# Optimization experiments

Measured on AMD Instinct MI355X. Metric: run time of the kernel, lower is better.

## Reference

```python
import jax, jax.numpy as jnp
import numpy as np
import math

N = 100000      # num nodes
D = 5           # fixed degree per node (<=5 -> exact Shapley enumeration path)
F_IN = 128
F_OUT = 128


def _subset_coeffs(d):
    """Exact Shapley subset-enumeration coefficients for a node with d neighbors.
    For subset S (mask m_k over neighbor slots, |S|=s):
      marginal = (sum_S + x_i)/(s+1) - (sum_S/s if s>0 else 0)   [since mean_S]
      weight   = s! (d-s)! / (d+1)!
    contrib = sum_k w_k*marginal_k = einsum(sum_S, c1) + x_i * sum(c2)
    """
    k = np.arange(2 ** d)
    masks = ((k[:, None] >> np.arange(d)) & 1).astype(np.float32)  # [2^d, d]
    s = masks.sum(axis=1)
    fact = np.vectorize(math.factorial)
    w = (fact(s.astype(np.int64)) * fact((d - s).astype(np.int64))
         / math.factorial(d + 1)).astype(np.float32)
    c1 = np.where(s > 0, w * (1.0 / (s + 1.0) - 1.0 / np.maximum(s, 1.0)), 0.0).astype(np.float32)
    c2 = (w / (s + 1.0)).astype(np.float32)
    return jnp.asarray(masks), jnp.asarray(c1), jnp.asarray(float(c2.sum()))


def setup_inputs() -> dict:
    key = jax.random.key(0)
    k1, k2, k3 = jax.random.split(key, 3)
    x = jax.random.normal(k1, (N, F_IN), dtype=jnp.float32)
    # fixed-degree graph: node i owns edges [i*D, (i+1)*D); row sorted
    row = jnp.repeat(jnp.arange(N, dtype=jnp.int32), D)
    col = jax.random.randint(k2, (N * D,), 0, N, dtype=jnp.int32)
    edge_index = jnp.stack([row, col])  # [2, N*D]
    W = jax.random.normal(k3, (F_OUT, F_IN), dtype=jnp.float32) / np.float32(np.sqrt(F_IN))
    return {"x": x, "edge_index": edge_index, "W": W}


def reference(x, edge_index, W):
    n = x.shape[0]
    col = edge_index[1]
    d = col.shape[0] // n
    nbrs = col.reshape(n, d)          # neighbors of node i (row is sorted, fixed degree)
    xn = x[nbrs]                      # [n, d, f] gathered neighbor features
    masks, c1, c2_sum = _subset_coeffs(d)
    # per-subset neighbor-feature sums: [n, 2^d, f]
    sum_S = jnp.einsum('kd,ndf->nkf', masks, xn)
    contrib = jnp.einsum('nkf,k->nf', sum_S, c1) + x * c2_sum
    shapley = x + contrib             # x_i + Shapley contribution
    out = jax.nn.relu(shapley @ W.T)  # Linear(bias=False) + relu
    return out
```

## Files before the change

kernel.cpp:

```cpp
#include <hip/hip_runtime.h>
#include <hip/hip_bf16.h>

typedef __attribute__((ext_vector_type(8))) short short8;
typedef __attribute__((ext_vector_type(4))) float f32x4;

#define DEG 5
#define FDIM 128
#define MT 64
#define NTHR 256
#define LROW 136

__device__ __forceinline__ short f2bf(float f) {
    unsigned u = __builtin_bit_cast(unsigned, f);
    unsigned r = (u + 0x7fffu + ((u >> 16) & 1u)) >> 16;
    return (short)(r & 0xffffu);
}

__global__ __launch_bounds__(NTHR) void shapley_gnn_kernel(
    const float* __restrict__ x,
    const int* __restrict__ col,
    const float* __restrict__ W,
    float* __restrict__ out,
    int n)
{
    __shared__ short sS[MT * LROW];
    __shared__ short sW[FDIM * LROW];
    __shared__ int sIdx[MT * DEG];

    const int tid = threadIdx.x;
    const int base = blockIdx.x * MT;

    for (int i = tid; i < MT * DEG; i += NTHR) {
        int e = base * DEG + i;
        sIdx[i] = (e < n * DEG) ? col[e] : 0;
    }

    for (int t = tid; t < FDIM * 16; t += NTHR) {
        int r = t >> 4;
        int c = t & 15;
        const float4* wp = reinterpret_cast<const float4*>(W + r * FDIM + c * 8);
        float4 w0 = wp[0];
        float4 w1 = wp[1];
        short8 v;
        v[0] = f2bf(w0.x); v[1] = f2bf(w0.y); v[2] = f2bf(w0.z); v[3] = f2bf(w0.w);
        v[4] = f2bf(w1.x); v[5] = f2bf(w1.y); v[6] = f2bf(w1.z); v[7] = f2bf(w1.w);
        *reinterpret_cast<short8*>(&sW[r * LROW + c * 8]) = v;
    }
    __syncthreads();

    const float CSELF = 1.4083333333333334f;
    const float ALPHA = -0.04833333333333333f;

    for (int t = tid; t < MT * 16; t += NTHR) {
        int m = t >> 4;
        int c = t & 15;
        int node = base + m;
        float a0, a1, a2, a3, a4, a5, a6, a7;
        if (node < n) {
            const float4* xp = reinterpret_cast<const float4*>(x + (size_t)node * FDIM + c * 8);
            float4 s0 = xp[0], s1 = xp[1];
            a0 = CSELF * s0.x; a1 = CSELF * s0.y; a2 = CSELF * s0.z; a3 = CSELF * s0.w;
            a4 = CSELF * s1.x; a5 = CSELF * s1.y; a6 = CSELF * s1.z; a7 = CSELF * s1.w;
            #pragma unroll
            for (int j = 0; j < DEG; ++j) {
                int nb = sIdx[m * DEG + j];
                const float4* np = reinterpret_cast<const float4*>(x + (size_t)nb * FDIM + c * 8);
                float4 b0 = np[0], b1 = np[1];
                a0 += ALPHA * b0.x; a1 += ALPHA * b0.y; a2 += ALPHA * b0.z; a3 += ALPHA * b0.w;
                a4 += ALPHA * b1.x; a5 += ALPHA * b1.y; a6 += ALPHA * b1.z; a7 += ALPHA * b1.w;
            }
        } else {
            a0 = a1 = a2 = a3 = a4 = a5 = a6 = a7 = 0.f;
        }
        short8 v;
        v[0] = f2bf(a0); v[1] = f2bf(a1); v[2] = f2bf(a2); v[3] = f2bf(a3);
        v[4] = f2bf(a4); v[5] = f2bf(a5); v[6] = f2bf(a6); v[7] = f2bf(a7);
        *reinterpret_cast<short8*>(&sS[m * LROW + c * 8]) = v;
    }
    __syncthreads();

    const int wave = tid >> 6;
    const int lane = tid & 63;
    const int lr = lane & 15;
    const int lg = lane >> 4;

    short8 afrag[4];
    const short* arow = &sS[(wave * 16 + lr) * LROW];
    #pragma unroll
    for (int kk = 0; kk < 4; ++kk)
        afrag[kk] = *reinterpret_cast<const short8*>(arow + kk * 32 + lg * 8);

    f32x4 acc[8];
    #pragma unroll
    for (int t = 0; t < 8; ++t) acc[t] = (f32x4){0.f, 0.f, 0.f, 0.f};

    #pragma unroll
    for (int t = 0; t < 8; ++t) {
        const short* brow = &sW[(t * 16 + lr) * LROW];
        #pragma unroll
        for (int kk = 0; kk < 4; ++kk) {
            short8 bfrag = *reinterpret_cast<const short8*>(brow + kk * 32 + lg * 8);
            acc[t] = __builtin_amdgcn_mfma_f32_16x16x32_bf16(afrag[kk], bfrag, acc[t], 0, 0, 0);
        }
    }

    #pragma unroll
    for (int t = 0; t < 8; ++t) {
        #pragma unroll
        for (int i = 0; i < 4; ++i) {
            int nrow = base + wave * 16 + lg * 4 + i;
            if (nrow < n) {
                float v = acc[t][i];
                out[(size_t)nrow * FDIM + t * 16 + lr] = v > 0.f ? v : 0.f;
            }
        }
    }
}

extern "C" void kernel_launch(void* const* d_in, const int* in_sizes, int n_in,
                              void* d_out, int out_size, void* d_ws, size_t ws_size,
                              hipStream_t stream) {
    const float* x  = (const float*)d_in[0];
    const int* ei   = (const int*)d_in[1];
    const float* W  = (const float*)d_in[2];
    float* out      = (float*)d_out;

    int n = in_sizes[0] / FDIM;
    const int* col = ei + (size_t)n * DEG;

    int blocks = (n + MT - 1) / MT;
    hipLaunchKernelGGL(shapley_gnn_kernel, dim3(blocks), dim3(NTHR), 0, stream,
                       x, col, W, out, n);
}
```

Baseline: 59.42 us.

## Pre-convert W to bf16 MFMA fragment layout in a prep kernel

Adds a small prep kernel that converts W to bf16 and stores it in workspace already arranged in the per-lane MFMA B-fragment order. The main kernel no longer stages and converts W into shared memory in every block. Instead each lane loads its B fragments straight from global memory (L2-resident, coalesced). This removes the redundant per-block W conversion and about 34KB of LDS per block, which may raise occupancy. In exchange it adds a second launch and global/L2 loads inside the MFMA loop.

New measurement: 60.75 us. +2.2%, slower.

```diff
diff --git a/kernel.cpp b/kernel.cpp
--- a/kernel.cpp
+++ b/kernel.cpp
@@ -16,15 +16,32 @@
     return (short)(r & 0xffffu);
 }
 
+__global__ __launch_bounds__(256) void prep_w_kernel(
+    const float* __restrict__ W, short* __restrict__ wswz)
+{
+    int t = blockIdx.x * 256 + threadIdx.x;
+    int frag = t >> 6;
+    int lane = t & 63;
+    int tt = frag >> 2;
+    int kk = frag & 3;
+    int lr = lane & 15;
+    int lg = lane >> 4;
+    const float4* wp = reinterpret_cast<const float4*>(W + (tt * 16 + lr) * FDIM + kk * 32 + lg * 8);
+    float4 w0 = wp[0], w1 = wp[1];
+    short8 v;
+    v[0] = f2bf(w0.x); v[1] = f2bf(w0.y); v[2] = f2bf(w0.z); v[3] = f2bf(w0.w);
+    v[4] = f2bf(w1.x); v[5] = f2bf(w1.y); v[6] = f2bf(w1.z); v[7] = f2bf(w1.w);
+    *reinterpret_cast<short8*>(wswz + (size_t)t * 8) = v;
+}
+
 __global__ __launch_bounds__(NTHR) void shapley_gnn_kernel(
     const float* __restrict__ x,
     const int* __restrict__ col,
-    const float* __restrict__ W,
+    const short* __restrict__ wswz,
     float* __restrict__ out,
     int n)
 {
     __shared__ short sS[MT * LROW];
-    __shared__ short sW[FDIM * LROW];
     __shared__ int sIdx[MT * DEG];
 
     const int tid = threadIdx.x;
@@ -33,18 +50,6 @@
     for (int i = tid; i < MT * DEG; i += NTHR) {
         int e = base * DEG + i;
         sIdx[i] = (e < n * DEG) ? col[e] : 0;
-    }
-
-    for (int t = tid; t < FDIM * 16; t += NTHR) {
-        int r = t >> 4;
-        int c = t & 15;
-        const float4* wp = reinterpret_cast<const float4*>(W + r * FDIM + c * 8);
-        float4 w0 = wp[0];
-        float4 w1 = wp[1];
-        short8 v;
-        v[0] = f2bf(w0.x); v[1] = f2bf(w0.y); v[2] = f2bf(w0.z); v[3] = f2bf(w0.w);
-        v[4] = f2bf(w1.x); v[5] = f2bf(w1.y); v[6] = f2bf(w1.z); v[7] = f2bf(w1.w);
-        *reinterpret_cast<short8*>(&sW[r * LROW + c * 8]) = v;
     }
     __syncthreads();
 
@@ -96,10 +101,10 @@
 
     #pragma unroll
     for (int t = 0; t < 8; ++t) {
-        const short* brow = &sW[(t * 16 + lr) * LROW];
         #pragma unroll
         for (int kk = 0; kk < 4; ++kk) {
-            short8 bfrag = *reinterpret_cast<const short8*>(brow + kk * 32 + lg * 8);
+            short8 bfrag = *reinterpret_cast<const short8*>(
+                wswz + (((size_t)(t * 4 + kk) * 64 + lane) * 8));
             acc[t] = __builtin_amdgcn_mfma_f32_16x16x32_bf16(afrag[kk], bfrag, acc[t], 0, 0, 0);
         }
     }
@@ -124,11 +129,14 @@
     const int* ei   = (const int*)d_in[1];
     const float* W  = (const float*)d_in[2];
     float* out      = (float*)d_out;
+    short* wswz     = (short*)d_ws;
 
     int n = in_sizes[0] / FDIM;
     const int* col = ei + (size_t)n * DEG;
 
+    hipLaunchKernelGGL(prep_w_kernel, dim3(8), dim3(256), 0, stream, W, wswz);
+
     int blocks = (n + MT - 1) / MT;
     hipLaunchKernelGGL(shapley_gnn_kernel, dim3(blocks), dim3(NTHR), 0, stream,
-                       x, col, W, out, n);
+                       x, col, wswz, out, n);
 }
```
